# Performance work log

Hardware: AMD Instinct MI355X
Metric: run time of the kernel (lower is better)

The kernel has to match this reference:

```python
import jax, jax.numpy as jnp
import numpy as np

B, S, D = 4, 4096, 1024

def setup_inputs() -> dict:
    key = jax.random.key(0)
    k1, k2, k3 = jax.random.split(key, 3)
    scale = 1.0 / np.sqrt(D)
    x = jax.random.normal(k1, (B, S, D), dtype=jnp.float32)
    W_qkv = jax.random.normal(k2, (3 * D, D), dtype=jnp.float32) * scale
    b_qkv = jnp.zeros((3 * D,), dtype=jnp.float32)
    W_gate = jax.random.normal(k3, (D, D), dtype=jnp.float32) * scale
    b_gate = jnp.zeros((D,), dtype=jnp.float32)
    return {"x": x, "W_qkv": W_qkv, "b_qkv": b_qkv, "W_gate": W_gate, "b_gate": b_gate}

def reference(x, W_qkv, b_qkv, W_gate, b_gate):
    # qkv projection: [B,S,3D]
    qkv = jnp.einsum('bsd,ed->bse', x, W_qkv) + b_qkv
    q, k, v = jnp.split(qkv, 3, axis=-1)  # each [B,S,D]
    # associative linear-attention state: running sum of k*v along seq
    kv_state = jnp.cumsum(k * v, axis=1)
    g = jax.nn.sigmoid(jnp.einsum('bsd,ed->bse', x, W_gate) + b_gate)
    return q * kv_state * g
```

## Files before the change

### kernel.cpp

```cpp
#include <hip/hip_runtime.h>
#include <hip/hip_bf16.h>

#define BB 4
#define SS 4096
#define DD 1024
#define MM (BB * SS)
#define KK DD
#define NN (4 * DD)

typedef __attribute__((ext_vector_type(8))) short bf16x8;
typedef __attribute__((ext_vector_type(4))) float f32x4;

__device__ __forceinline__ unsigned short f2bf(float f) {
  unsigned u = __float_as_uint(f);
  u += 0x7FFF + ((u >> 16) & 1);
  return (unsigned short)(u >> 16);
}
__device__ __forceinline__ float bf2f(unsigned short h) {
  return __uint_as_float(((unsigned)h) << 16);
}

__global__ __launch_bounds__(256) void k_convert(const float* __restrict__ src,
                                                 unsigned short* __restrict__ dst, int n4) {
  int i = blockIdx.x * blockDim.x + threadIdx.x;
  int stride = gridDim.x * blockDim.x;
  for (; i < n4; i += stride) {
    float4 v = reinterpret_cast<const float4*>(src)[i];
    ushort4 o;
    o.x = f2bf(v.x); o.y = f2bf(v.y); o.z = f2bf(v.z); o.w = f2bf(v.w);
    reinterpret_cast<ushort4*>(dst)[i] = o;
  }
}

#define BM 128
#define BN 128
#define BKSTEP 64

__global__ __launch_bounds__(256, 2) void k_gemm(const unsigned short* __restrict__ A,
                                                 const unsigned short* __restrict__ Bw,
                                                 unsigned short* __restrict__ C,
                                                 const float* __restrict__ bqkv,
                                                 const float* __restrict__ bgate) {
  __shared__ unsigned short As[BM * BKSTEP];
  __shared__ unsigned short Bs[BN * BKSTEP];

  const int bid = blockIdx.x;
  const int tn = bid & 31;
  const int tm = bid >> 5;
  const int m0 = tm * BM, n0 = tn * BN;

  const int tid = threadIdx.x;
  const int wave = tid >> 6;
  const int lane = tid & 63;
  const int wm = wave >> 1, wn = wave & 1;

  const int r = lane & 15;
  const int kgrp = (lane >> 4) * 8;

  f32x4 acc[4][4] = {};

  for (int k0 = 0; k0 < KK; k0 += BKSTEP) {
#pragma unroll
    for (int inst = 0; inst < 4; ++inst) {
      int o = wave * 4096 + inst * 1024 + lane * 16;
      int row = o >> 7;
      int cb = o & 127;
      const char* ga = (const char*)A + ((size_t)(m0 + row) * KK + k0) * 2 + cb;
      const char* gb = (const char*)Bw + ((size_t)(n0 + row) * KK + k0) * 2 + cb;
      __builtin_amdgcn_global_load_lds(
          (const __attribute__((address_space(1))) void*)ga,
          (__attribute__((address_space(3))) void*)((char*)As + wave * 4096 + inst * 1024),
          16, 0, 0);
      __builtin_amdgcn_global_load_lds(
          (const __attribute__((address_space(1))) void*)gb,
          (__attribute__((address_space(3))) void*)((char*)Bs + wave * 4096 + inst * 1024),
          16, 0, 0);
    }
    __syncthreads();

#pragma unroll
    for (int kk = 0; kk < BKSTEP; kk += 32) {
      bf16x8 af[4], bfr[4];
#pragma unroll
      for (int i = 0; i < 4; ++i)
        af[i] = *reinterpret_cast<const bf16x8*>(&As[(wm * 64 + i * 16 + r) * BKSTEP + kk + kgrp]);
#pragma unroll
      for (int j = 0; j < 4; ++j)
        bfr[j] = *reinterpret_cast<const bf16x8*>(&Bs[(wn * 64 + j * 16 + r) * BKSTEP + kk + kgrp]);
#pragma unroll
      for (int i = 0; i < 4; ++i)
#pragma unroll
        for (int j = 0; j < 4; ++j)
          acc[i][j] = __builtin_amdgcn_mfma_f32_16x16x32_bf16(af[i], bfr[j], acc[i][j], 0, 0, 0);
    }
    __syncthreads();
  }

#pragma unroll
  for (int j = 0; j < 4; ++j) {
    int col = n0 + wn * 64 + j * 16 + r;
    float bias = (col < 3 * DD) ? bqkv[col] : bgate[col - 3 * DD];
#pragma unroll
    for (int i = 0; i < 4; ++i) {
      int row0 = m0 + wm * 64 + i * 16 + ((lane >> 4) << 2);
      f32x4 v = acc[i][j];
#pragma unroll
      for (int q = 0; q < 4; ++q)
        C[(size_t)(row0 + q) * NN + col] = f2bf(v[q] + bias);
    }
  }
}

#define NCH 128
#define CSZ (SS / NCH)

__global__ __launch_bounds__(256) void k_pass1(const unsigned short* __restrict__ C,
                                               float* __restrict__ part) {
  int b = blockIdx.x >> 7;
  int c = blockIdx.x & (NCH - 1);
  int d = threadIdx.x * 4;
  float a0 = 0.f, a1 = 0.f, a2 = 0.f, a3 = 0.f;
  for (int s = c * CSZ; s < (c + 1) * CSZ; ++s) {
    size_t rowb = (size_t)(b * SS + s) * NN;
    ushort4 k4 = *(const ushort4*)&C[rowb + DD + d];
    ushort4 v4 = *(const ushort4*)&C[rowb + 2 * DD + d];
    a0 += bf2f(k4.x) * bf2f(v4.x);
    a1 += bf2f(k4.y) * bf2f(v4.y);
    a2 += bf2f(k4.z) * bf2f(v4.z);
    a3 += bf2f(k4.w) * bf2f(v4.w);
  }
  float4 o = {a0, a1, a2, a3};
  *(float4*)&part[(size_t)(b * NCH + c) * DD + d] = o;
}

__global__ __launch_bounds__(256) void k_pass2(float* __restrict__ part) {
  int g = blockIdx.x * blockDim.x + threadIdx.x;
  int b = g >> 10;
  int d = g & (DD - 1);
  float run = 0.f;
  for (int c = 0; c < NCH; ++c) {
    size_t idx = (size_t)(b * NCH + c) * DD + d;
    float t = part[idx];
    part[idx] = run;
    run += t;
  }
}

__global__ __launch_bounds__(256) void k_pass3(const unsigned short* __restrict__ C,
                                               const float* __restrict__ part,
                                               float* __restrict__ out) {
  int b = blockIdx.x >> 7;
  int c = blockIdx.x & (NCH - 1);
  int d = threadIdx.x * 4;
  float4 a = *(const float4*)&part[(size_t)(b * NCH + c) * DD + d];
  for (int s = c * CSZ; s < (c + 1) * CSZ; ++s) {
    size_t rowb = (size_t)(b * SS + s) * NN;
    ushort4 q4 = *(const ushort4*)&C[rowb + d];
    ushort4 k4 = *(const ushort4*)&C[rowb + DD + d];
    ushort4 v4 = *(const ushort4*)&C[rowb + 2 * DD + d];
    ushort4 g4 = *(const ushort4*)&C[rowb + 3 * DD + d];
    a.x += bf2f(k4.x) * bf2f(v4.x);
    a.y += bf2f(k4.y) * bf2f(v4.y);
    a.z += bf2f(k4.z) * bf2f(v4.z);
    a.w += bf2f(k4.w) * bf2f(v4.w);
    float4 o;
    o.x = bf2f(q4.x) * a.x / (1.f + __expf(-bf2f(g4.x)));
    o.y = bf2f(q4.y) * a.y / (1.f + __expf(-bf2f(g4.y)));
    o.z = bf2f(q4.z) * a.z / (1.f + __expf(-bf2f(g4.z)));
    o.w = bf2f(q4.w) * a.w / (1.f + __expf(-bf2f(g4.w)));
    *(float4*)&out[(size_t)(b * SS + s) * DD + d] = o;
  }
}

extern "C" void kernel_launch(void* const* d_in, const int* in_sizes, int n_in,
                              void* d_out, int out_size, void* d_ws, size_t ws_size,
                              hipStream_t stream) {
  const float* x = (const float*)d_in[0];
  const float* Wqkv = (const float*)d_in[1];
  const float* bqkv = (const float*)d_in[2];
  const float* Wgate = (const float*)d_in[3];
  const float* bgate = (const float*)d_in[4];
  float* out = (float*)d_out;

  char* ws = (char*)d_ws;
  unsigned short* xb = (unsigned short*)ws;
  unsigned short* wb = (unsigned short*)(ws + (size_t)33554432);
  unsigned short* Cc = (unsigned short*)(ws + (size_t)41943040);
  float* part = (float*)(ws + (size_t)176160768);

  k_convert<<<2048, 256, 0, stream>>>(x, xb, MM * KK / 4);
  k_convert<<<1024, 256, 0, stream>>>(Wqkv, wb, 3 * DD * DD / 4);
  k_convert<<<256, 256, 0, stream>>>(Wgate, wb + 3 * DD * DD, DD * DD / 4);

  k_gemm<<<(MM / BM) * (NN / BN), 256, 0, stream>>>(xb, wb, Cc, bqkv, bgate);

  k_pass1<<<BB * NCH, 256, 0, stream>>>(Cc, part);
  k_pass2<<<16, 256, 0, stream>>>(part);
  k_pass3<<<BB * NCH, 256, 0, stream>>>(Cc, part, out);
}
```

Measured before the change: 339.7 us.

## Rewrite GEMM with 256x256 pipelined tiles and fuse k*v and sigmoid into epilogue

```diff
diff --git a/kernel.cpp b/kernel.cpp
--- a/kernel.cpp
+++ b/kernel.cpp
@@ -32,111 +32,216 @@
   }
 }
 
-#define BM 128
-#define BN 128
-#define BKSTEP 64
-
-__global__ __launch_bounds__(256, 2) void k_gemm(const unsigned short* __restrict__ A,
-                                                 const unsigned short* __restrict__ Bw,
-                                                 unsigned short* __restrict__ C,
-                                                 const float* __restrict__ bqkv,
-                                                 const float* __restrict__ bgate) {
-  __shared__ unsigned short As[BM * BKSTEP];
-  __shared__ unsigned short Bs[BN * BKSTEP];
-
-  const int bid = blockIdx.x;
-  const int tn = bid & 31;
-  const int tm = bid >> 5;
-  const int m0 = tm * BM, n0 = tn * BN;
-
-  const int tid = threadIdx.x;
-  const int wave = tid >> 6;
-  const int lane = tid & 63;
-  const int wm = wave >> 1, wn = wave & 1;
-
-  const int r = lane & 15;
-  const int kgrp = (lane >> 4) * 8;
-
-  f32x4 acc[4][4] = {};
-
-  for (int k0 = 0; k0 < KK; k0 += BKSTEP) {
-#pragma unroll
-    for (int inst = 0; inst < 4; ++inst) {
-      int o = wave * 4096 + inst * 1024 + lane * 16;
-      int row = o >> 7;
-      int cb = o & 127;
-      const char* ga = (const char*)A + ((size_t)(m0 + row) * KK + k0) * 2 + cb;
-      const char* gb = (const char*)Bw + ((size_t)(n0 + row) * KK + k0) * 2 + cb;
-      __builtin_amdgcn_global_load_lds(
-          (const __attribute__((address_space(1))) void*)ga,
-          (__attribute__((address_space(3))) void*)((char*)As + wave * 4096 + inst * 1024),
-          16, 0, 0);
-      __builtin_amdgcn_global_load_lds(
-          (const __attribute__((address_space(1))) void*)gb,
-          (__attribute__((address_space(3))) void*)((char*)Bs + wave * 4096 + inst * 1024),
-          16, 0, 0);
+__global__ __launch_bounds__(256) void k_convert_wperm(const float* __restrict__ Wqkv,
+                                                       const float* __restrict__ Wgate,
+                                                       unsigned short* __restrict__ dst) {
+  int n = blockIdx.x;
+  const float* src;
+  if (n < 1024) {
+    src = Wqkv + (size_t)n * 1024;
+  } else if (n < 3072) {
+    int t = (n - 1024) >> 4;
+    int d = ((t >> 1) << 4) + (n & 15);
+    src = Wqkv + (size_t)(1024 + ((t & 1) << 10) + d) * 1024;
+  } else {
+    src = Wgate + (size_t)(n - 3072) * 1024;
+  }
+  unsigned short* o = dst + (size_t)n * 1024;
+  int i = threadIdx.x * 4;
+  float4 v = *(const float4*)(src + i);
+  ushort4 u;
+  u.x = f2bf(v.x); u.y = f2bf(v.y); u.z = f2bf(v.z); u.w = f2bf(v.w);
+  *(ushort4*)(o + i) = u;
+}
+
+#define BAR() do { asm volatile("" ::: "memory"); __builtin_amdgcn_s_barrier(); asm volatile("" ::: "memory"); } while (0)
+#define VMW2() asm volatile("s_waitcnt vmcnt(2)" ::: "memory")
+#define VMW0() asm volatile("s_waitcnt vmcnt(0)" ::: "memory")
+
+__global__ __launch_bounds__(512, 2) void k_gemm2(const unsigned short* __restrict__ A,
+                                                  const unsigned short* __restrict__ W,
+                                                  unsigned short* __restrict__ Qd,
+                                                  unsigned short* __restrict__ KVd,
+                                                  unsigned short* __restrict__ Gd,
+                                                  const float* __restrict__ bqkv,
+                                                  const float* __restrict__ bgate) {
+  __shared__ unsigned short sm[32768];
+
+  int bid0 = blockIdx.x;
+  int bid = (bid0 & 7) * 128 + (bid0 >> 3);
+  int tn = bid & 15, tm = bid >> 4;
+  int m0 = tm * 256, n0 = tn * 256;
+
+  int tid = threadIdx.x, wave = tid >> 6, lane = tid & 63;
+  int wm = wave >> 2, wn = wave & 3;
+  int r = lane & 15, g = lane >> 4;
+
+  const unsigned short* Ag = A + (size_t)(m0 + (tid >> 2)) * KK + (tid & 3) * 8;
+  const unsigned short* Wg = W + (size_t)(n0 + (tid >> 2)) * KK + (tid & 3) * 8;
+
+  int aoff = wm * 4096 + r * 32 + g * 8;
+  int boff = 16384 + (wn >> 1) * 4096 + ((wn & 1) * 64 + r) * 32 + g * 8;
+
+#define STAGE_A(t, h, d)                                                              \
+  __builtin_amdgcn_global_load_lds(                                                   \
+      (const __attribute__((address_space(1))) void*)(Ag + (size_t)(h)*131072 + (t)*32), \
+      (__attribute__((address_space(3))) void*)(&sm[(d)*8192 + (h)*4096 + wave * 512]), \
+      16, 0, 0)
+#define STAGE_B(t, h, d)                                                              \
+  __builtin_amdgcn_global_load_lds(                                                   \
+      (const __attribute__((address_space(1))) void*)(Wg + (size_t)(h)*131072 + (t)*32), \
+      (__attribute__((address_space(3))) void*)(&sm[16384 + (d)*8192 + (h)*4096 + wave * 512]), \
+      16, 0, 0)
+#define LDA(m, d) (*reinterpret_cast<const bf16x8*>(&sm[aoff + (d)*8192 + (m)*512]))
+#define LDB(n, d) (*reinterpret_cast<const bf16x8*>(&sm[boff + (d)*8192 + (n)*512]))
+#define MFMA(x, y, c) c = __builtin_amdgcn_mfma_f32_16x16x32_bf16(x, y, c, 0, 0, 0)
+
+  STAGE_A(0, 0, 0); STAGE_A(0, 1, 0);
+  STAGE_B(0, 0, 0); STAGE_B(0, 1, 0);
+  STAGE_A(1, 0, 1); STAGE_A(1, 1, 1);
+  VMW2();
+  BAR();
+
+  f32x4 acc[8][4] = {};
+  bf16x8 a[8], bb0, bb1;
+
+  for (int i = 0; i < 15; ++i) {
+    int t0 = 2 * i;
+#pragma unroll
+    for (int m = 0; m < 8; ++m) a[m] = LDA(m, 0);
+    bb0 = LDB(0, 0); bb1 = LDB(1, 0);
+    STAGE_B(t0 + 1, 0, 1); STAGE_B(t0 + 1, 1, 1);
+    BAR();
+    __builtin_amdgcn_s_setprio(1);
+#pragma unroll
+    for (int m = 0; m < 8; ++m) { MFMA(a[m], bb0, acc[m][0]); MFMA(a[m], bb1, acc[m][1]); }
+    __builtin_amdgcn_s_setprio(0);
+    BAR();
+    bb0 = LDB(2, 0); bb1 = LDB(3, 0);
+    STAGE_A(t0 + 2, 0, 0); STAGE_A(t0 + 2, 1, 0);
+    BAR();
+    __builtin_amdgcn_s_setprio(1);
+#pragma unroll
+    for (int m = 0; m < 8; ++m) { MFMA(a[m], bb0, acc[m][2]); MFMA(a[m], bb1, acc[m][3]); }
+    __builtin_amdgcn_s_setprio(0);
+    VMW2();
+    BAR();
+#pragma unroll
+    for (int m = 0; m < 8; ++m) a[m] = LDA(m, 1);
+    bb0 = LDB(0, 1); bb1 = LDB(1, 1);
+    STAGE_B(t0 + 2, 0, 0); STAGE_B(t0 + 2, 1, 0);
+    BAR();
+    __builtin_amdgcn_s_setprio(1);
+#pragma unroll
+    for (int m = 0; m < 8; ++m) { MFMA(a[m], bb0, acc[m][0]); MFMA(a[m], bb1, acc[m][1]); }
+    __builtin_amdgcn_s_setprio(0);
+    BAR();
+    bb0 = LDB(2, 1); bb1 = LDB(3, 1);
+    STAGE_A(t0 + 3, 0, 1); STAGE_A(t0 + 3, 1, 1);
+    BAR();
+    __builtin_amdgcn_s_setprio(1);
+#pragma unroll
+    for (int m = 0; m < 8; ++m) { MFMA(a[m], bb0, acc[m][2]); MFMA(a[m], bb1, acc[m][3]); }
+    __builtin_amdgcn_s_setprio(0);
+    VMW2();
+    BAR();
+  }
+
+#pragma unroll
+  for (int m = 0; m < 8; ++m) a[m] = LDA(m, 0);
+  bb0 = LDB(0, 0); bb1 = LDB(1, 0);
+  STAGE_B(31, 0, 1); STAGE_B(31, 1, 1);
+  BAR();
+#pragma unroll
+  for (int m = 0; m < 8; ++m) { MFMA(a[m], bb0, acc[m][0]); MFMA(a[m], bb1, acc[m][1]); }
+  BAR();
+  bb0 = LDB(2, 0); bb1 = LDB(3, 0);
+  BAR();
+#pragma unroll
+  for (int m = 0; m < 8; ++m) { MFMA(a[m], bb0, acc[m][2]); MFMA(a[m], bb1, acc[m][3]); }
+  VMW0();
+  BAR();
+#pragma unroll
+  for (int m = 0; m < 8; ++m) a[m] = LDA(m, 1);
+  bb0 = LDB(0, 1); bb1 = LDB(1, 1);
+  BAR();
+#pragma unroll
+  for (int m = 0; m < 8; ++m) { MFMA(a[m], bb0, acc[m][0]); MFMA(a[m], bb1, acc[m][1]); }
+  BAR();
+  bb0 = LDB(2, 1); bb1 = LDB(3, 1);
+  BAR();
+#pragma unroll
+  for (int m = 0; m < 8; ++m) { MFMA(a[m], bb0, acc[m][2]); MFMA(a[m], bb1, acc[m][3]); }
+
+  int growb = m0 + wm * 128 + g * 4;
+  if (tn < 4) {
+#pragma unroll
+    for (int n = 0; n < 4; ++n) {
+      int col = n0 + wn * 64 + n * 16 + r;
+      float bias = bqkv[col];
+#pragma unroll
+      for (int m = 0; m < 8; ++m)
+#pragma unroll
+        for (int q = 0; q < 4; ++q)
+          Qd[(size_t)(growb + m * 16 + q) * DD + col] = f2bf(acc[m][n][q] + bias);
     }
-    __syncthreads();
-
-#pragma unroll
-    for (int kk = 0; kk < BKSTEP; kk += 32) {
-      bf16x8 af[4], bfr[4];
-#pragma unroll
-      for (int i = 0; i < 4; ++i)
-        af[i] = *reinterpret_cast<const bf16x8*>(&As[(wm * 64 + i * 16 + r) * BKSTEP + kk + kgrp]);
-#pragma unroll
-      for (int j = 0; j < 4; ++j)
-        bfr[j] = *reinterpret_cast<const bf16x8*>(&Bs[(wn * 64 + j * 16 + r) * BKSTEP + kk + kgrp]);
-#pragma unroll
-      for (int i = 0; i < 4; ++i)
-#pragma unroll
-        for (int j = 0; j < 4; ++j)
-          acc[i][j] = __builtin_amdgcn_mfma_f32_16x16x32_bf16(af[i], bfr[j], acc[i][j], 0, 0, 0);
+  } else if (tn < 12) {
+    int cb = n0 - 1024 + wn * 64;
+#pragma unroll
+    for (int np = 0; np < 2; ++np) {
+      int d = (cb >> 1) + np * 16 + r;
+      float bk = bqkv[1024 + d], bv = bqkv[2048 + d];
+#pragma unroll
+      for (int m = 0; m < 8; ++m)
+#pragma unroll
+        for (int q = 0; q < 4; ++q) {
+          float kvv = (acc[m][2 * np][q] + bk) * (acc[m][2 * np + 1][q] + bv);
+          KVd[(size_t)(growb + m * 16 + q) * DD + d] = f2bf(kvv);
+        }
     }
-    __syncthreads();
-  }
-
-#pragma unroll
-  for (int j = 0; j < 4; ++j) {
-    int col = n0 + wn * 64 + j * 16 + r;
-    float bias = (col < 3 * DD) ? bqkv[col] : bgate[col - 3 * DD];
-#pragma unroll
-    for (int i = 0; i < 4; ++i) {
-      int row0 = m0 + wm * 64 + i * 16 + ((lane >> 4) << 2);
-      f32x4 v = acc[i][j];
-#pragma unroll
-      for (int q = 0; q < 4; ++q)
-        C[(size_t)(row0 + q) * NN + col] = f2bf(v[q] + bias);
+  } else {
+    int cb0 = n0 - 3072;
+#pragma unroll
+    for (int n = 0; n < 4; ++n) {
+      int c = cb0 + wn * 64 + n * 16 + r;
+      float bias = bgate[c];
+#pragma unroll
+      for (int m = 0; m < 8; ++m)
+#pragma unroll
+        for (int q = 0; q < 4; ++q) {
+          float gv = acc[m][n][q] + bias;
+          Gd[(size_t)(growb + m * 16 + q) * DD + c] = f2bf(1.f / (1.f + __expf(-gv)));
+        }
     }
   }
+#undef STAGE_A
+#undef STAGE_B
+#undef LDA
+#undef LDB
+#undef MFMA
 }
 
 #define NCH 128
 #define CSZ (SS / NCH)
 
-__global__ __launch_bounds__(256) void k_pass1(const unsigned short* __restrict__ C,
+__global__ __launch_bounds__(256) void k_pass1(const unsigned short* __restrict__ KV,
                                                float* __restrict__ part) {
   int b = blockIdx.x >> 7;
   int c = blockIdx.x & (NCH - 1);
   int d = threadIdx.x * 4;
   float a0 = 0.f, a1 = 0.f, a2 = 0.f, a3 = 0.f;
   for (int s = c * CSZ; s < (c + 1) * CSZ; ++s) {
-    size_t rowb = (size_t)(b * SS + s) * NN;
-    ushort4 k4 = *(const ushort4*)&C[rowb + DD + d];
-    ushort4 v4 = *(const ushort4*)&C[rowb + 2 * DD + d];
-    a0 += bf2f(k4.x) * bf2f(v4.x);
-    a1 += bf2f(k4.y) * bf2f(v4.y);
-    a2 += bf2f(k4.z) * bf2f(v4.z);
-    a3 += bf2f(k4.w) * bf2f(v4.w);
+    ushort4 kv = *(const ushort4*)&KV[(size_t)(b * SS + s) * DD + d];
+    a0 += bf2f(kv.x); a1 += bf2f(kv.y); a2 += bf2f(kv.z); a3 += bf2f(kv.w);
   }
   float4 o = {a0, a1, a2, a3};
   *(float4*)&part[(size_t)(b * NCH + c) * DD + d] = o;
 }
 
 __global__ __launch_bounds__(256) void k_pass2(float* __restrict__ part) {
-  int g = blockIdx.x * blockDim.x + threadIdx.x;
-  int b = g >> 10;
-  int d = g & (DD - 1);
+  int gg = blockIdx.x * blockDim.x + threadIdx.x;
+  int b = gg >> 10;
+  int d = gg & (DD - 1);
   float run = 0.f;
   for (int c = 0; c < NCH; ++c) {
     size_t idx = (size_t)(b * NCH + c) * DD + d;
@@ -146,7 +251,9 @@
   }
 }
 
-__global__ __launch_bounds__(256) void k_pass3(const unsigned short* __restrict__ C,
+__global__ __launch_bounds__(256) void k_pass3(const unsigned short* __restrict__ Q,
+                                               const unsigned short* __restrict__ KV,
+                                               const unsigned short* __restrict__ G,
                                                const float* __restrict__ part,
                                                float* __restrict__ out) {
   int b = blockIdx.x >> 7;
@@ -154,21 +261,17 @@
   int d = threadIdx.x * 4;
   float4 a = *(const float4*)&part[(size_t)(b * NCH + c) * DD + d];
   for (int s = c * CSZ; s < (c + 1) * CSZ; ++s) {
-    size_t rowb = (size_t)(b * SS + s) * NN;
-    ushort4 q4 = *(const ushort4*)&C[rowb + d];
-    ushort4 k4 = *(const ushort4*)&C[rowb + DD + d];
-    ushort4 v4 = *(const ushort4*)&C[rowb + 2 * DD + d];
-    ushort4 g4 = *(const ushort4*)&C[rowb + 3 * DD + d];
-    a.x += bf2f(k4.x) * bf2f(v4.x);
-    a.y += bf2f(k4.y) * bf2f(v4.y);
-    a.z += bf2f(k4.z) * bf2f(v4.z);
-    a.w += bf2f(k4.w) * bf2f(v4.w);
+    size_t rowb = (size_t)(b * SS + s) * DD;
+    ushort4 q4 = *(const ushort4*)&Q[rowb + d];
+    ushort4 kv4 = *(const ushort4*)&KV[rowb + d];
+    ushort4 g4 = *(const ushort4*)&G[rowb + d];
+    a.x += bf2f(kv4.x); a.y += bf2f(kv4.y); a.z += bf2f(kv4.z); a.w += bf2f(kv4.w);
     float4 o;
-    o.x = bf2f(q4.x) * a.x / (1.f + __expf(-bf2f(g4.x)));
-    o.y = bf2f(q4.y) * a.y / (1.f + __expf(-bf2f(g4.y)));
-    o.z = bf2f(q4.z) * a.z / (1.f + __expf(-bf2f(g4.z)));
-    o.w = bf2f(q4.w) * a.w / (1.f + __expf(-bf2f(g4.w)));
-    *(float4*)&out[(size_t)(b * SS + s) * DD + d] = o;
+    o.x = bf2f(q4.x) * a.x * bf2f(g4.x);
+    o.y = bf2f(q4.y) * a.y * bf2f(g4.y);
+    o.z = bf2f(q4.z) * a.z * bf2f(g4.z);
+    o.w = bf2f(q4.w) * a.w * bf2f(g4.w);
+    *(float4*)&out[rowb + d] = o;
   }
 }
 
@@ -185,16 +288,17 @@
   char* ws = (char*)d_ws;
   unsigned short* xb = (unsigned short*)ws;
   unsigned short* wb = (unsigned short*)(ws + (size_t)33554432);
-  unsigned short* Cc = (unsigned short*)(ws + (size_t)41943040);
-  float* part = (float*)(ws + (size_t)176160768);
+  unsigned short* Qd = (unsigned short*)(ws + (size_t)41943040);
+  unsigned short* KVd = (unsigned short*)(ws + (size_t)75497472);
+  unsigned short* Gd = (unsigned short*)(ws + (size_t)109051904);
+  float* part = (float*)(ws + (size_t)142606336);
 
   k_convert<<<2048, 256, 0, stream>>>(x, xb, MM * KK / 4);
-  k_convert<<<1024, 256, 0, stream>>>(Wqkv, wb, 3 * DD * DD / 4);
-  k_convert<<<256, 256, 0, stream>>>(Wgate, wb + 3 * DD * DD, DD * DD / 4);
-
-  k_gemm<<<(MM / BM) * (NN / BN), 256, 0, stream>>>(xb, wb, Cc, bqkv, bgate);
-
-  k_pass1<<<BB * NCH, 256, 0, stream>>>(Cc, part);
+  k_convert_wperm<<<4096, 256, 0, stream>>>(Wqkv, Wgate, wb);
+
+  k_gemm2<<<1024, 512, 0, stream>>>(xb, wb, Qd, KVd, Gd, bqkv, bgate);
+
+  k_pass1<<<BB * NCH, 256, 0, stream>>>(KVd, part);
   k_pass2<<<16, 256, 0, stream>>>(part);
-  k_pass3<<<BB * NCH, 256, 0, stream>>>(Cc, part, out);
-}
+  k_pass3<<<BB * NCH, 256, 0, stream>>>(Qd, KVd, Gd, part, out);
+}
```

After: 326.6 us. -3.9%, faster.
